# Optimization experiments

Measured on AMD Instinct MI355X. Metric: run time of the kernel, lower is better.

The kernel has to match this reference:

```python
import jax, jax.numpy as jnp
import numpy as np

SMPL_PARENT = np.array([0,0,0,1,2,3,4,5,6,7,8,9,9,9,12,13,14,16,17,18,19,20,21], dtype=np.int64)

def quat2mat(quat):
    # quat: [N,4] (w,x,y,z) -> [N,3,3]
    q = quat / jnp.linalg.norm(quat, axis=1, keepdims=True)
    w, x, y, z = q[:, 0], q[:, 1], q[:, 2], q[:, 3]
    w2, x2, y2, z2 = w*w, x*x, y*y, z*z
    wx, wy, wz = w*x, w*y, w*z
    xy, xz, yz = x*y, x*z, y*z
    R = jnp.stack([w2+x2-y2-z2, 2*xy-2*wz, 2*wy+2*xz,
                   2*wz+2*xy, w2-x2+y2-z2, 2*yz-2*wx,
                   2*xz-2*wy, 2*wx+2*yz, w2-x2-y2+z2], axis=1)
    return R.reshape(-1, 3, 3)

def rodrigues(theta):
    # theta: [N,3] axis-angle -> [N,3,3]
    angle = jnp.linalg.norm(theta + 1e-8, axis=1, keepdims=True)
    normalized = theta / angle
    half = angle * 0.5
    quat = jnp.concatenate([jnp.cos(half), jnp.sin(half) * normalized], axis=1)
    return quat2mat(quat)

def setup_inputs() -> dict:
    key = jax.random.key(0)
    ks = jax.random.split(key, 8)
    B, V = 64, 50000
    pose = jax.random.normal(ks[0], (B, 72), dtype=jnp.float32) * 0.3
    beta = jax.random.normal(ks[1], (B, 300), dtype=jnp.float32) * 0.03
    v_template = jax.random.normal(ks[2], (V, 3), dtype=jnp.float32)
    shapedirs = jax.random.normal(ks[3], (V, 3, 300), dtype=jnp.float32) * 0.01
    posedirs = jax.random.normal(ks[4], (V, 3, 207), dtype=jnp.float32) * 0.01
    Jr = jax.random.uniform(ks[5], (24, V), dtype=jnp.float32)
    J_regressor = Jr / jnp.sum(Jr, axis=1, keepdims=True)
    w = jax.random.uniform(ks[6], (V, 24), dtype=jnp.float32)
    weights = w / jnp.sum(w, axis=1, keepdims=True)
    parent = jnp.asarray(SMPL_PARENT)
    return {"pose": pose, "beta": beta, "v_template": v_template,
            "shapedirs": shapedirs, "posedirs": posedirs,
            "J_regressor": J_regressor, "weights": weights, "parent": parent}

def reference(pose, beta, v_template, shapedirs, posedirs, J_regressor, weights, parent):
    B = pose.shape[0]
    parent_np = np.asarray(jax.device_get(parent))
    # shape blendshapes: [B,V,3]
    v_shaped = jnp.einsum('vds,bs->bvd', shapedirs, beta) + v_template[None]
    J = jnp.einsum('jv,bvd->bjd', J_regressor, v_shaped)
    # pose -> rotation matrices [B,24,3,3]
    R = rodrigues(pose.reshape(-1, 3)).reshape(B, 24, 3, 3)
    lrotmin = (R[:, 1:] - jnp.eye(3, dtype=R.dtype)).reshape(B, 207)
    # pose blendshapes
    v_posed = v_shaped + jnp.einsum('vdp,bp->bvd', posedirs, lrotmin)
    # relative joint locations
    J_rel = J.at[:, 1:].set(J[:, 1:] - J[:, parent_np])
    # local transforms [B,24,4,4]
    G_top = jnp.concatenate([R, J_rel[..., None]], axis=-1)  # [B,24,3,4]
    pad = jnp.broadcast_to(jnp.array([0., 0., 0., 1.], dtype=R.dtype), (B, 24, 1, 4))
    G_local = jnp.concatenate([G_top, pad], axis=2)
    # kinematic chain (24 structurally-distinct joints)
    Gs = [G_local[:, 0]]
    for i in range(1, 24):
        Gs.append(jnp.matmul(Gs[parent_np[i - 1]], G_local[:, i]))
    G = jnp.stack(Gs, axis=1)  # [B,24,4,4]
    # remove rest-pose translation: G[...,:,3] -= G @ [J,0]
    rest4 = jnp.concatenate([J, jnp.zeros((B, 24, 1), dtype=J.dtype)], axis=2)  # [B,24,4]
    corr = jnp.einsum('bjmn,bjn->bjm', G, rest4)
    G = G.at[..., :, 3].add(-corr)
    # LBS: per-vertex transform [B,V,4,4]
    T = jnp.einsum('vj,bjmn->bvmn', weights, G)
    v_h = jnp.concatenate([v_posed, jnp.ones_like(v_posed[..., :1])], axis=-1)  # [B,V,4]
    v = jnp.einsum('bvmn,bvn->bvm', T, v_h)[..., :3]
    return v
```

## Files before the change

### kernel.cpp

```cpp
#include <hip/hip_runtime.h>
#include <math.h>

#define NV 50000
#define NM 150000

__constant__ int c_par[24]   = {0, 0,0,0, 1,2,3, 4,5,6, 7,8,9,9,9, 12,13,14, 16,17, 18,19, 20,21};
__constant__ int c_depth[24] = {0, 1,1,1, 2,2,2, 3,3,3, 4,4,4,4,4, 5,5,5, 6,6, 7,7, 8,8};

__global__ __launch_bounds__(256)
void prep_kernel(const float* __restrict__ beta, float* __restrict__ betaT,
                 float* __restrict__ J)
{
    int i = blockIdx.x * 256 + threadIdx.x;
    if (i < 300 * 64) {
        int k = i >> 6, b = i & 63;
        betaT[i] = beta[b * 300 + k];
    }
    if (i < 64 * 24 * 3) J[i] = 0.f;
}

template<int K, int MODE>
__global__ __launch_bounds__(128)
void gemm_kernel(const float* __restrict__ A, const float* __restrict__ Bt,
                 const float* __restrict__ add, float* __restrict__ C)
{
    __shared__ float As[64 * 33];
    const int t    = threadIdx.x;
    const int row0 = blockIdx.x * 64;
    const int lrow = t & 63;
    const int half = __builtin_amdgcn_readfirstlane(t >> 6);
    const int row  = row0 + lrow;

    float acc[32];
    #pragma unroll
    for (int b = 0; b < 32; ++b) acc[b] = 0.f;

    const int srow = t >> 3;
    const int skg  = t & 7;

    const int nfull = K / 32;
    for (int c = 0; c < nfull; ++c) {
        const int k0 = c * 32;
        __syncthreads();
        #pragma unroll
        for (int p = 0; p < 4; ++p) {
            int r = p * 16 + srow;
            float4 v = make_float4(0.f, 0.f, 0.f, 0.f);
            if (row0 + r < NM)
                v = *(const float4*)(A + (size_t)(row0 + r) * K + k0 + skg * 4);
            float* d = As + r * 33 + skg * 4;
            d[0] = v.x; d[1] = v.y; d[2] = v.z; d[3] = v.w;
        }
        __syncthreads();
        #pragma unroll 4
        for (int k = 0; k < 32; ++k) {
            float a = As[lrow * 33 + k];
            const float* Bk = Bt + (size_t)(k0 + k) * 64 + half * 32;
            #pragma unroll
            for (int b = 0; b < 32; ++b) acc[b] = fmaf(Bk[b], a, acc[b]);
        }
    }
    const int krem = K - nfull * 32;
    if (krem > 0) {
        const int k0 = nfull * 32;
        __syncthreads();
        #pragma unroll
        for (int p = 0; p < 4; ++p) {
            int r = p * 16 + srow;
            #pragma unroll
            for (int q = 0; q < 4; ++q) {
                int k = skg * 4 + q;
                float v = 0.f;
                if (k < krem && row0 + r < NM)
                    v = A[(size_t)(row0 + r) * K + k0 + k];
                As[r * 33 + k] = v;
            }
        }
        __syncthreads();
        for (int k = 0; k < krem; ++k) {
            float a = As[lrow * 33 + k];
            const float* Bk = Bt + (size_t)(k0 + k) * 64 + half * 32;
            #pragma unroll
            for (int b = 0; b < 32; ++b) acc[b] = fmaf(Bk[b], a, acc[b]);
        }
    }

    if (row >= NM) return;
    if constexpr (MODE == 0) {
        float t0 = add[row];
        float* dst = C + (size_t)row * 64 + half * 32;
        #pragma unroll
        for (int q = 0; q < 8; ++q) {
            float4 v = {acc[q*4+0] + t0, acc[q*4+1] + t0, acc[q*4+2] + t0, acc[q*4+3] + t0};
            *(float4*)(dst + q * 4) = v;
        }
    } else {
        const float* av = add + (size_t)row * 64 + half * 32;
        #pragma unroll
        for (int b = 0; b < 32; ++b)
            C[(size_t)(half * 32 + b) * NM + row] = acc[b] + av[b];
    }
}

__global__ __launch_bounds__(512)
void jreduce_kernel(const float* __restrict__ vs, const float* __restrict__ Jr,
                    float* J)
{
    __shared__ float Ls[4][64][73];
    const int t = threadIdx.x;
    const int b = t & 63;
    const int w = __builtin_amdgcn_readfirstlane(t >> 6);

    float acc[24][3];
    #pragma unroll
    for (int j = 0; j < 24; ++j) { acc[j][0]=0.f; acc[j][1]=0.f; acc[j][2]=0.f; }

    const int v0 = blockIdx.x * 200 + w * 25;
    #pragma unroll 5
    for (int v = v0; v < v0 + 25; ++v) {
        float p0 = vs[(size_t)(v*3+0)*64 + b];
        float p1 = vs[(size_t)(v*3+1)*64 + b];
        float p2 = vs[(size_t)(v*3+2)*64 + b];
        #pragma unroll
        for (int j = 0; j < 24; ++j) {
            float r = Jr[(size_t)j*NV + v];
            acc[j][0] += r*p0; acc[j][1] += r*p1; acc[j][2] += r*p2;
        }
    }

    if (w < 4) {
        float* d = Ls[w][b];
        #pragma unroll
        for (int j = 0; j < 24; ++j) {
            d[j*3+0] = acc[j][0]; d[j*3+1] = acc[j][1]; d[j*3+2] = acc[j][2];
        }
    }
    __syncthreads();
    if (w >= 4) {
        float* d = Ls[w-4][b];
        #pragma unroll
        for (int j = 0; j < 24; ++j) {
            d[j*3+0] += acc[j][0]; d[j*3+1] += acc[j][1]; d[j*3+2] += acc[j][2];
        }
    }
    __syncthreads();

    #pragma unroll
    for (int q = 0; q < 9; ++q) {
        int oid = t * 9 + q;
        int bb = oid / 72, c = oid - bb * 72;
        float s = Ls[0][bb][c] + Ls[1][bb][c] + Ls[2][bb][c] + Ls[3][bb][c];
        atomicAdd(&J[(size_t)bb * 72 + c], s);
    }
}

__global__ __launch_bounds__(192)
void pose_kernel(const float* __restrict__ pose, const float* __restrict__ J,
                 float* __restrict__ G, float* __restrict__ lrotT)
{
    __shared__ float Gl[8][24][12];
    __shared__ float Gc[8][24][12];
    const int t  = threadIdx.x;
    const int bl = t / 24;
    const int j  = t % 24;
    const int b  = blockIdx.x * 8 + bl;

    float tx = pose[b*72 + j*3 + 0];
    float ty = pose[b*72 + j*3 + 1];
    float tz = pose[b*72 + j*3 + 2];
    float ax = tx + 1e-8f, ay = ty + 1e-8f, az = tz + 1e-8f;
    float angle = sqrtf(ax*ax + ay*ay + az*az);
    float nx = tx / angle, ny = ty / angle, nz = tz / angle;
    float half = 0.5f * angle;
    float sw = sinf(half);
    float qw = cosf(half), qx = sw*nx, qy = sw*ny, qz = sw*nz;
    float qn = sqrtf(qw*qw + qx*qx + qy*qy + qz*qz);
    qw /= qn; qx /= qn; qy /= qn; qz /= qn;
    float w2=qw*qw, x2=qx*qx, y2=qy*qy, z2=qz*qz;
    float xy=qx*qy, xz=qx*qz, yz=qy*qz, wx=qw*qx, wy=qw*qy, wz=qw*qz;
    float r00 = w2+x2-y2-z2, r01 = 2.f*(xy-wz), r02 = 2.f*(wy+xz);
    float r10 = 2.f*(wz+xy), r11 = w2-x2+y2-z2, r12 = 2.f*(yz-wx);
    float r20 = 2.f*(xz-wy), r21 = 2.f*(wx+yz), r22 = w2-x2-y2+z2;

    if (j >= 1) {
        const int k9 = (j-1)*9;
        lrotT[(size_t)(k9+0)*64+b]=r00-1.f; lrotT[(size_t)(k9+1)*64+b]=r01;
        lrotT[(size_t)(k9+2)*64+b]=r02;     lrotT[(size_t)(k9+3)*64+b]=r10;
        lrotT[(size_t)(k9+4)*64+b]=r11-1.f; lrotT[(size_t)(k9+5)*64+b]=r12;
        lrotT[(size_t)(k9+6)*64+b]=r20;     lrotT[(size_t)(k9+7)*64+b]=r21;
        lrotT[(size_t)(k9+8)*64+b]=r22-1.f;
    }
    float jx = J[(size_t)(b*24+j)*3+0];
    float jy = J[(size_t)(b*24+j)*3+1];
    float jz = J[(size_t)(b*24+j)*3+2];
    float rx = jx, ry = jy, rz = jz;
    if (j > 0) {
        int p = c_par[j];
        rx -= J[(size_t)(b*24+p)*3+0];
        ry -= J[(size_t)(b*24+p)*3+1];
        rz -= J[(size_t)(b*24+p)*3+2];
    }
    float* gl = Gl[bl][j];
    gl[0]=r00; gl[1]=r01; gl[2]=r02;  gl[3]=rx;
    gl[4]=r10; gl[5]=r11; gl[6]=r12;  gl[7]=ry;
    gl[8]=r20; gl[9]=r21; gl[10]=r22; gl[11]=rz;
    __syncthreads();

    if (j == 0) {
        #pragma unroll
        for (int c = 0; c < 12; ++c) Gc[bl][0][c] = Gl[bl][0][c];
    }
    const int dj = c_depth[j];
    for (int lvl = 1; lvl <= 8; ++lvl) {
        __syncthreads();
        if (dj == lvl) {
            const float* Aa = Gc[bl][c_par[j]];
            const float* Bb = Gl[bl][j];
            float* D = Gc[bl][j];
            #pragma unroll
            for (int r = 0; r < 3; ++r) {
                float a0=Aa[r*4+0], a1=Aa[r*4+1], a2=Aa[r*4+2], a3=Aa[r*4+3];
                D[r*4+0] = a0*Bb[0] + a1*Bb[4] + a2*Bb[8];
                D[r*4+1] = a0*Bb[1] + a1*Bb[5] + a2*Bb[9];
                D[r*4+2] = a0*Bb[2] + a1*Bb[6] + a2*Bb[10];
                D[r*4+3] = a0*Bb[3] + a1*Bb[7] + a2*Bb[11] + a3;
            }
        }
    }
    __syncthreads();

    const float* Gi = Gc[bl][j];
    float* go = G + (size_t)(b*24 + j) * 12;
    #pragma unroll
    for (int r = 0; r < 3; ++r) {
        go[r*4+0] = Gi[r*4+0];
        go[r*4+1] = Gi[r*4+1];
        go[r*4+2] = Gi[r*4+2];
        go[r*4+3] = Gi[r*4+3] - (Gi[r*4+0]*jx + Gi[r*4+1]*jy + Gi[r*4+2]*jz);
    }
}

__global__ __launch_bounds__(256)
void skin_kernel(const float* __restrict__ vp, const float* __restrict__ G,
                 const float* __restrict__ wts, float* __restrict__ out)
{
    const int v = blockIdx.x * 256 + threadIdx.x;
    if (v >= NV) return;
    const int b0 = blockIdx.y * 8;
    float w[24];
    const float4* wp = (const float4*)(wts + (size_t)v * 24);
    #pragma unroll
    for (int q = 0; q < 6; ++q) {
        float4 t = wp[q];
        w[q*4+0]=t.x; w[q*4+1]=t.y; w[q*4+2]=t.z; w[q*4+3]=t.w;
    }
    for (int b = b0; b < b0 + 8; ++b) {
        const float* pb = vp + (size_t)b * NM + v*3;
        float px = pb[0], py = pb[1], pz = pb[2];
        float ox = 0.f, oy = 0.f, oz = 0.f;
        const float* Gb = G + (size_t)b * 24 * 12;
        #pragma unroll
        for (int j = 0; j < 24; ++j) {
            const float* g = Gb + j*12;
            float wj = w[j];
            ox += wj * (g[0]*px + g[1]*py + g[2]*pz  + g[3]);
            oy += wj * (g[4]*px + g[5]*py + g[6]*pz  + g[7]);
            oz += wj * (g[8]*px + g[9]*py + g[10]*pz + g[11]);
        }
        float* ob = out + (size_t)b * NM + v*3;
        ob[0] = ox; ob[1] = oy; ob[2] = oz;
    }
}

extern "C" void kernel_launch(void* const* d_in, const int* in_sizes, int n_in,
                              void* d_out, int out_size, void* d_ws, size_t ws_size,
                              hipStream_t stream) {
    const float* pose       = (const float*)d_in[0];
    const float* beta       = (const float*)d_in[1];
    const float* v_template = (const float*)d_in[2];
    const float* shapedirs  = (const float*)d_in[3];
    const float* posedirs   = (const float*)d_in[4];
    const float* Jreg       = (const float*)d_in[5];
    const float* weights    = (const float*)d_in[6];
    float* out = (float*)d_out;

    char* ws = (char*)d_ws;
    float* vs_ws    = (float*)(ws);
    float* vp_ws    = (float*)(ws + 38400000);
    float* betaT_ws = (float*)(ws + 38400000);
    float* J_ws     = (float*)(ws + 76800000);
    float* G_ws     = (float*)(ws + 76818432);
    float* lrotT_ws = (float*)(ws + 76892160);

    prep_kernel<<<75, 256, 0, stream>>>(beta, betaT_ws, J_ws);
    gemm_kernel<300, 0><<<2344, 128, 0, stream>>>(shapedirs, betaT_ws, v_template, vs_ws);
    jreduce_kernel<<<250, 512, 0, stream>>>(vs_ws, Jreg, J_ws);
    pose_kernel<<<8, 192, 0, stream>>>(pose, J_ws, G_ws, lrotT_ws);
    gemm_kernel<207, 1><<<2344, 128, 0, stream>>>(posedirs, lrotT_ws, vs_ws, vp_ws);
    skin_kernel<<<dim3(196, 8), 256, 0, stream>>>(vp_ws, G_ws, weights, out);
}
```

Baseline: 628.4 us.

## Replace FP32 scalar GEMMs with bf16 MFMA matrix-core kernels

```diff
diff --git a/kernel.cpp b/kernel.cpp
--- a/kernel.cpp
+++ b/kernel.cpp
@@ -3,6 +3,10 @@
 
 #define NV 50000
 #define NM 150000
+
+typedef float  f32x4  __attribute__((ext_vector_type(4)));
+typedef __bf16 bf16x8 __attribute__((ext_vector_type(8)));
+typedef float  f4u    __attribute__((ext_vector_type(4), aligned(4)));
 
 __constant__ int c_par[24]   = {0, 0,0,0, 1,2,3, 4,5,6, 7,8,9,9,9, 12,13,14, 16,17, 18,19, 20,21};
 __constant__ int c_depth[24] = {0, 1,1,1, 2,2,2, 3,3,3, 4,4,4,4,4, 5,5,5, 6,6, 7,7, 8,8};
@@ -20,85 +24,88 @@
 }
 
 template<int K, int MODE>
-__global__ __launch_bounds__(128)
-void gemm_kernel(const float* __restrict__ A, const float* __restrict__ Bt,
-                 const float* __restrict__ add, float* __restrict__ C)
-{
-    __shared__ float As[64 * 33];
+__global__ __launch_bounds__(512)
+void gemm_mfma(const float* __restrict__ A, const float* __restrict__ Bt,
+               const float* __restrict__ add, float* __restrict__ C)
+{
+    constexpr int NFULL = K / 32;
+    constexpr int NC    = (K + 31) / 32;
+    constexpr int PB    = NC * 32 + 8;
+    __shared__ __bf16 Bs[64 * PB];
+
     const int t    = threadIdx.x;
-    const int row0 = blockIdx.x * 64;
-    const int lrow = t & 63;
-    const int half = __builtin_amdgcn_readfirstlane(t >> 6);
-    const int row  = row0 + lrow;
-
-    float acc[32];
-    #pragma unroll
-    for (int b = 0; b < 32; ++b) acc[b] = 0.f;
-
-    const int srow = t >> 3;
-    const int skg  = t & 7;
-
-    const int nfull = K / 32;
-    for (int c = 0; c < nfull; ++c) {
-        const int k0 = c * 32;
-        __syncthreads();
-        #pragma unroll
-        for (int p = 0; p < 4; ++p) {
-            int r = p * 16 + srow;
-            float4 v = make_float4(0.f, 0.f, 0.f, 0.f);
-            if (row0 + r < NM)
-                v = *(const float4*)(A + (size_t)(row0 + r) * K + k0 + skg * 4);
-            float* d = As + r * 33 + skg * 4;
-            d[0] = v.x; d[1] = v.y; d[2] = v.z; d[3] = v.w;
-        }
-        __syncthreads();
-        #pragma unroll 4
-        for (int k = 0; k < 32; ++k) {
-            float a = As[lrow * 33 + k];
-            const float* Bk = Bt + (size_t)(k0 + k) * 64 + half * 32;
+    const int row0 = blockIdx.x * 128;
+    const int w    = __builtin_amdgcn_readfirstlane(t >> 6);
+    const int l    = t & 63;
+    const int lr   = l & 15;
+    const int kb   = l >> 4;
+
+    for (int i = t; i < 64 * NC * 32; i += 512) {
+        int k = i >> 6, n = i & 63;
+        float v = (k < K) ? Bt[(size_t)k * 64 + n] : 0.f;
+        Bs[n * PB + k] = (__bf16)v;
+    }
+    __syncthreads();
+
+    const int grow = row0 + w * 16 + lr;
+    const int arow = grow < NM ? grow : NM - 1;
+    const float* Arow = A + (size_t)arow * K;
+
+    f32x4 acc[4] = {};
+    float cur[8], nxt[8];
+    {
+        f4u p0 = *(const f4u*)(Arow + kb * 8);
+        f4u p1 = *(const f4u*)(Arow + kb * 8 + 4);
+        cur[0]=p0.x; cur[1]=p0.y; cur[2]=p0.z; cur[3]=p0.w;
+        cur[4]=p1.x; cur[5]=p1.y; cur[6]=p1.z; cur[7]=p1.w;
+    }
+    #pragma unroll
+    for (int c = 0; c < NC; ++c) {
+        if (c + 1 < NC) {
+            const int kn = (c + 1) * 32 + kb * 8;
+            if (c + 1 < NFULL) {
+                f4u p0 = *(const f4u*)(Arow + kn);
+                f4u p1 = *(const f4u*)(Arow + kn + 4);
+                nxt[0]=p0.x; nxt[1]=p0.y; nxt[2]=p0.z; nxt[3]=p0.w;
+                nxt[4]=p1.x; nxt[5]=p1.y; nxt[6]=p1.z; nxt[7]=p1.w;
+            } else {
+                #pragma unroll
+                for (int e = 0; e < 8; ++e)
+                    nxt[e] = (kn + e < K) ? Arow[kn + e] : 0.f;
+            }
+        }
+        bf16x8 af;
+        #pragma unroll
+        for (int e = 0; e < 8; ++e) af[e] = (__bf16)cur[e];
+        #pragma unroll
+        for (int n = 0; n < 4; ++n) {
+            const bf16x8 bfv = *(const bf16x8*)(Bs + (n * 16 + lr) * PB + c * 32 + kb * 8);
+            if constexpr (MODE == 0)
+                acc[n] = __builtin_amdgcn_mfma_f32_16x16x32_bf16(af, bfv, acc[n], 0, 0, 0);
+            else
+                acc[n] = __builtin_amdgcn_mfma_f32_16x16x32_bf16(bfv, af, acc[n], 0, 0, 0);
+        }
+        #pragma unroll
+        for (int e = 0; e < 8; ++e) cur[e] = nxt[e];
+    }
+
+    if (row0 + w * 16 >= NM) return;
+    if constexpr (MODE == 0) {
+        f4u ta = *(const f4u*)(add + row0 + w * 16 + kb * 4);
+        #pragma unroll
+        for (int n = 0; n < 4; ++n)
             #pragma unroll
-            for (int b = 0; b < 32; ++b) acc[b] = fmaf(Bk[b], a, acc[b]);
-        }
-    }
-    const int krem = K - nfull * 32;
-    if (krem > 0) {
-        const int k0 = nfull * 32;
-        __syncthreads();
-        #pragma unroll
-        for (int p = 0; p < 4; ++p) {
-            int r = p * 16 + srow;
+            for (int r = 0; r < 4; ++r)
+                C[(size_t)(row0 + w * 16 + kb * 4 + r) * 64 + n * 16 + lr] = acc[n][r] + ta[r];
+    } else {
+        const size_t vrow = row0 + w * 16 + lr;
+        #pragma unroll
+        for (int m = 0; m < 4; ++m) {
+            f4u av = *(const f4u*)(add + vrow * 64 + m * 16 + kb * 4);
             #pragma unroll
-            for (int q = 0; q < 4; ++q) {
-                int k = skg * 4 + q;
-                float v = 0.f;
-                if (k < krem && row0 + r < NM)
-                    v = A[(size_t)(row0 + r) * K + k0 + k];
-                As[r * 33 + k] = v;
-            }
-        }
-        __syncthreads();
-        for (int k = 0; k < krem; ++k) {
-            float a = As[lrow * 33 + k];
-            const float* Bk = Bt + (size_t)(k0 + k) * 64 + half * 32;
-            #pragma unroll
-            for (int b = 0; b < 32; ++b) acc[b] = fmaf(Bk[b], a, acc[b]);
-        }
-    }
-
-    if (row >= NM) return;
-    if constexpr (MODE == 0) {
-        float t0 = add[row];
-        float* dst = C + (size_t)row * 64 + half * 32;
-        #pragma unroll
-        for (int q = 0; q < 8; ++q) {
-            float4 v = {acc[q*4+0] + t0, acc[q*4+1] + t0, acc[q*4+2] + t0, acc[q*4+3] + t0};
-            *(float4*)(dst + q * 4) = v;
-        }
-    } else {
-        const float* av = add + (size_t)row * 64 + half * 32;
-        #pragma unroll
-        for (int b = 0; b < 32; ++b)
-            C[(size_t)(half * 32 + b) * NM + row] = acc[b] + av[b];
+            for (int r = 0; r < 4; ++r)
+                C[(size_t)(m * 16 + kb * 4 + r) * NM + vrow] = acc[m][r] + av[r];
+        }
     }
 }
 
@@ -293,9 +300,9 @@
     float* lrotT_ws = (float*)(ws + 76892160);
 
     prep_kernel<<<75, 256, 0, stream>>>(beta, betaT_ws, J_ws);
-    gemm_kernel<300, 0><<<2344, 128, 0, stream>>>(shapedirs, betaT_ws, v_template, vs_ws);
+    gemm_mfma<300, 0><<<1172, 512, 0, stream>>>(shapedirs, betaT_ws, v_template, vs_ws);
     jreduce_kernel<<<250, 512, 0, stream>>>(vs_ws, Jreg, J_ws);
     pose_kernel<<<8, 192, 0, stream>>>(pose, J_ws, G_ws, lrotT_ws);
-    gemm_kernel<207, 1><<<2344, 128, 0, stream>>>(posedirs, lrotT_ws, vs_ws, vp_ws);
+    gemm_mfma<207, 1><<<1172, 512, 0, stream>>>(posedirs, lrotT_ws, vs_ws, vp_ws);
     skin_kernel<<<dim3(196, 8), 256, 0, stream>>>(vp_ws, G_ws, weights, out);
 }
```

Measured after the change: 606.3 us. -3.5%, faster.
